# Optimization experiments

Hardware: AMD Instinct MI355X
Metric: run time of the kernel (lower is better)

Reference implementation:

```python
import jax, jax.numpy as jnp
import numpy as np

SEQ, D_IN, D_OUT = 8192, 768, 64


def setup_inputs() -> dict:
    key = jax.random.key(0)
    k0, k1, k2, k3 = jax.random.split(key, 4)
    x = jax.random.normal(k0, (SEQ, D_IN), dtype=jnp.float32)
    # nn.Linear default init ~ U(-1/sqrt(d_in), 1/sqrt(d_in)); small scale keeps softmax stable
    s = 0.02
    Wq = jax.random.normal(k1, (D_IN, D_OUT), dtype=jnp.float32) * s
    Wk = jax.random.normal(k2, (D_IN, D_OUT), dtype=jnp.float32) * s
    Wv = jax.random.normal(k3, (D_IN, D_OUT), dtype=jnp.float32) * s
    return {"x": x, "Wq": Wq, "Wk": Wk, "Wv": Wv}


def reference(x, Wq, Wk, Wv):
    # queries/keys/values: [S, d_out]
    q = x @ Wq
    k = x @ Wk
    v = x @ Wv
    d_k = k.shape[-1]
    scores = q @ k.T / jnp.sqrt(jnp.asarray(d_k, x.dtype))  # [S, S]
    weights = jax.nn.softmax(scores, axis=-1)
    return weights @ v  # [S, d_out]
```

## Files before the change

### kernel.cpp

```cpp
#include <hip/hip_runtime.h>
#include <hip/hip_bf16.h>

#define SEQ  8192
#define DIN  768
#define DOUT 64

typedef __attribute__((ext_vector_type(8))) short short8;
typedef __attribute__((ext_vector_type(4))) short s16x4;
typedef __attribute__((ext_vector_type(4))) float f32x4;

__device__ inline unsigned short f2bf(float f) {
    __hip_bfloat16 h = __float2bfloat16(f);
    return __builtin_bit_cast(unsigned short, h);
}

__global__ __launch_bounds__(256) void wconv_kernel(
    const float* __restrict__ Wq, const float* __restrict__ Wk,
    const float* __restrict__ Wv, unsigned short* __restrict__ Wf) {
    int idx = blockIdx.x * 256 + threadIdx.x;
    int c = idx / DIN;
    int k = idx - c * DIN;
    int sel = c >> 6, cc = c & 63;
    const float* W = (sel == 0) ? Wq : ((sel == 1) ? Wk : Wv);
    float v = W[k * DOUT + cc];
    if (sel == 0) v *= 0.125f * 1.4426950408889634f;
    int nt = c >> 4, l15 = c & 15;
    int kt = k >> 6, k6 = k & 63;
    int h  = k6 >> 5, r5 = k6 & 31, g = r5 >> 3, e = r5 & 7;
    Wf[(((kt * 12 + nt) * 2 + h) << 9) + (g << 7) + (l15 << 3) + e] = f2bf(v);
}

__global__ __launch_bounds__(256) void proj_kernel(
    const float* __restrict__ x, const unsigned short* __restrict__ Wf,
    unsigned short* __restrict__ Q8, unsigned short* __restrict__ Kf,
    unsigned short* __restrict__ Vf) {
    __shared__ unsigned short xs[2][16 * 72];

    const int tid  = threadIdx.x;
    const int m0   = blockIdx.x * 16;
    const int lane = tid & 63;
    const int w    = tid >> 6;
    const int g    = lane >> 4;
    const int l15  = lane & 15;
    const int sr   = tid >> 4;
    const int sc4  = (tid & 15) * 4;

    f32x4 zero = {0.f, 0.f, 0.f, 0.f};
    f32x4 acc[3] = {zero, zero, zero};

    {
        float4 f = *reinterpret_cast<const float4*>(&x[(m0 + sr) * DIN + sc4]);
        s16x4 o4;
        o4[0] = (short)f2bf(f.x); o4[1] = (short)f2bf(f.y);
        o4[2] = (short)f2bf(f.z); o4[3] = (short)f2bf(f.w);
        *(s16x4*)&xs[0][sr * 72 + sc4] = o4;
    }
    __syncthreads();

    for (int kt = 0; kt < 12; ++kt) {
        const int cur = kt & 1;
        short8 a0 = *(short8*)&xs[cur][l15 * 72 + g * 8];
        short8 a1 = *(short8*)&xs[cur][l15 * 72 + g * 8 + 32];
        if (kt + 1 < 12) {
            float4 f = *reinterpret_cast<const float4*>(
                &x[(m0 + sr) * DIN + (kt + 1) * 64 + sc4]);
            s16x4 o4;
            o4[0] = (short)f2bf(f.x); o4[1] = (short)f2bf(f.y);
            o4[2] = (short)f2bf(f.z); o4[3] = (short)f2bf(f.w);
            *(s16x4*)&xs[cur ^ 1][sr * 72 + sc4] = o4;
        }
#pragma unroll
        for (int i = 0; i < 3; ++i) {
            int nt = w * 3 + i;
            const unsigned short* wb = &Wf[((kt * 12 + nt) * 2) * 512 + lane * 8];
            short8 b0 = *(const short8*)wb;
            short8 b1 = *(const short8*)(wb + 512);
            acc[i] = __builtin_amdgcn_mfma_f32_16x16x32_bf16(a0, b0, acc[i], 0, 0, 0);
            acc[i] = __builtin_amdgcn_mfma_f32_16x16x32_bf16(a1, b1, acc[i], 0, 0, 0);
        }
        __syncthreads();
    }
#pragma unroll
    for (int i = 0; i < 3; ++i) {
#pragma unroll
        for (int r = 0; r < 4; ++r) {
            int row = m0 + g * 4 + r;
            int col = (w * 3 + i) * 16 + l15;
            unsigned short b = f2bf(acc[i][r]);
            if (col < 64) {
                Q8[row * 64 + col] = b;
            } else if (col < 128) {
                int d  = col - 64;
                int t  = row >> 6, nt = (row >> 4) & 3, lk = row & 15;
                int h  = d >> 5, kg = (d >> 3) & 3, e = d & 7;
                Kf[(((t * 4 + nt) * 2 + h) * 64 + kg * 16 + lk) * 8 + e] = b;
            } else {
                int d  = col - 128;
                int kv = row;
                int t  = kv >> 6, k6 = kv & 63;
                int c  = k6 >> 5, r5 = k6 & 31;
                int hf = r5 >> 4, vg = (r5 >> 2) & 3, j = (r5 & 3) + hf * 4;
                int dn = d >> 4, lv = d & 15;
                Vf[(((t * 2 + c) * 4 + dn) * 64 + vg * 16 + lv) * 8 + j] = b;
            }
        }
    }
}

__global__ __launch_bounds__(256, 2) void flash_kernel(
    const unsigned short* __restrict__ Q8, const unsigned short* __restrict__ Kf,
    const unsigned short* __restrict__ Vf, float* __restrict__ Op,
    float* __restrict__ Lp, int ntiles) {
    const int tid  = threadIdx.x;
    const int w    = tid >> 6;
    const int lane = tid & 63;
    const int g    = lane >> 4;
    const int l15  = lane & 15;
    const int q0   = (blockIdx.x * 4 + w) * 64;
    const int nsub = ntiles * 2;
    const int sub0 = blockIdx.y * nsub;

    short8 qa[8];
#pragma unroll
    for (int qg = 0; qg < 4; ++qg) {
        qa[qg * 2 + 0] = *(const short8*)&Q8[(q0 + qg * 16 + l15) * 64 + g * 8];
        qa[qg * 2 + 1] = *(const short8*)&Q8[(q0 + qg * 16 + l15) * 64 + g * 8 + 32];
    }

    short8 onesf;
#pragma unroll
    for (int j = 0; j < 8; ++j) onesf[j] = (short)0x3F80;

    f32x4 zero = {0.f, 0.f, 0.f, 0.f};
    f32x4 o[4][4];
    f32x4 oL[4] = {zero, zero, zero, zero};
#pragma unroll
    for (int qg = 0; qg < 4; ++qg)
#pragma unroll
        for (int dn = 0; dn < 4; ++dn) o[qg][dn] = zero;

    const unsigned short* kfp = Kf + (size_t)sub0 * 2048 + lane * 8;
    const unsigned short* vfp = Vf + (size_t)sub0 * 2048 + lane * 8;

    short8 kb[2][2], vA[4], vB[4];
#pragma unroll
    for (int nt = 0; nt < 2; ++nt)
#pragma unroll
        for (int h = 0; h < 2; ++h)
            kb[nt][h] = *(const short8*)&kfp[(nt * 2 + h) * 512];
#pragma unroll
    for (int dn = 0; dn < 4; ++dn)
        vA[dn] = *(const short8*)&vfp[dn * 512];

#define FLASH_STEP(I, VCUR, VNXT)                                                            \
    {                                                                                        \
        f32x4 s[4][2];                                                                       \
        _Pragma("unroll")                                                                    \
        for (int qg = 0; qg < 4; ++qg)                                                       \
            _Pragma("unroll")                                                                \
            for (int nt = 0; nt < 2; ++nt) s[qg][nt] = zero;                                 \
        _Pragma("unroll")                                                                    \
        for (int nt = 0; nt < 2; ++nt)                                                       \
            _Pragma("unroll")                                                                \
            for (int qg = 0; qg < 4; ++qg) {                                                 \
                s[qg][nt] = __builtin_amdgcn_mfma_f32_16x16x32_bf16(kb[nt][0], qa[qg * 2 + 0], s[qg][nt], 0, 0, 0); \
                s[qg][nt] = __builtin_amdgcn_mfma_f32_16x16x32_bf16(kb[nt][1], qa[qg * 2 + 1], s[qg][nt], 0, 0, 0); \
            }                                                                                \
        if ((I) + 1 < nsub) {                                                                \
            _Pragma("unroll")                                                                \
            for (int nt = 0; nt < 2; ++nt)                                                   \
                _Pragma("unroll")                                                            \
                for (int h = 0; h < 2; ++h)                                                  \
                    kb[nt][h] = *(const short8*)&kfp[(size_t)((I) + 1) * 2048 + (nt * 2 + h) * 512]; \
            _Pragma("unroll")                                                                \
            for (int dn = 0; dn < 4; ++dn)                                                   \
                VNXT[dn] = *(const short8*)&vfp[(size_t)((I) + 1) * 2048 + dn * 512];        \
        }                                                                                    \
        short8 pa[4];                                                                        \
        _Pragma("unroll")                                                                    \
        for (int qg = 0; qg < 4; ++qg) {                                                     \
            float p[8];                                                                      \
            _Pragma("unroll")                                                                \
            for (int nt = 0; nt < 2; ++nt)                                                   \
                _Pragma("unroll")                                                            \
                for (int r = 0; r < 4; ++r)                                                  \
                    p[nt * 4 + r] = __builtin_amdgcn_exp2f(s[qg][nt][r]);                    \
            short8 pk;                                                                       \
            _Pragma("unroll")                                                                \
            for (int j = 0; j < 8; ++j) pk[j] = (short)f2bf(p[j]);                           \
            pa[qg] = pk;                                                                     \
        }                                                                                    \
        _Pragma("unroll")                                                                    \
        for (int qg = 0; qg < 4; ++qg)                                                       \
            oL[qg] = __builtin_amdgcn_mfma_f32_16x16x32_bf16(onesf, pa[qg], oL[qg], 0, 0, 0); \
        _Pragma("unroll")                                                                    \
        for (int dn = 0; dn < 4; ++dn)                                                       \
            _Pragma("unroll")                                                                \
            for (int qg = 0; qg < 4; ++qg)                                                   \
                o[qg][dn] = __builtin_amdgcn_mfma_f32_16x16x32_bf16(VCUR[dn], pa[qg], o[qg][dn], 0, 0, 0); \
    }

    for (int i = 0; i < nsub; i += 2) {
        FLASH_STEP(i, vA, vB)
        FLASH_STEP(i + 1, vB, vA)
    }
#undef FLASH_STEP

    const size_t sb = (size_t)blockIdx.y * SEQ;
#pragma unroll
    for (int qg = 0; qg < 4; ++qg) {
#pragma unroll
        for (int dn = 0; dn < 4; ++dn)
            *(f32x4*)&Op[(sb + q0 + qg * 16 + l15) * 64 + dn * 16 + 4 * g] = o[qg][dn];
        if (g == 0) {
            Lp[sb + q0 + qg * 16 + l15] = oL[qg][0];
        }
    }
}

__global__ __launch_bounds__(256) void reduce_kernel(
    const float* __restrict__ Op, const float* __restrict__ Lp,
    float* __restrict__ Out, int NS) {
    int q  = blockIdx.x * 16 + (threadIdx.x >> 4);
    int d4 = (threadIdx.x & 15) * 4;
    float L = 0.f;
    f32x4 acc = {0.f, 0.f, 0.f, 0.f};
    for (int s = 0; s < NS; ++s) {
        L   += Lp[s * SEQ + q];
        acc += *(const f32x4*)&Op[((size_t)s * SEQ + q) * 64 + d4];
    }
    float inv = 1.0f / L;
    f32x4 r = {acc[0] * inv, acc[1] * inv, acc[2] * inv, acc[3] * inv};
    *(f32x4*)&Out[q * 64 + d4] = r;
}

extern "C" void kernel_launch(void* const* d_in, const int* in_sizes, int n_in,
                              void* d_out, int out_size, void* d_ws, size_t ws_size,
                              hipStream_t stream) {
    const float* x  = (const float*)d_in[0];
    const float* Wq = (const float*)d_in[1];
    const float* Wk = (const float*)d_in[2];
    const float* Wv = (const float*)d_in[3];
    float* out = (float*)d_out;

    char* ws = (char*)d_ws;
    unsigned short* Wf = (unsigned short*)(ws);
    unsigned short* Q8 = (unsigned short*)(ws + 294912);
    unsigned short* Kf = (unsigned short*)(ws + 294912 + 1048576);
    unsigned short* Vf = (unsigned short*)(ws + 294912 + 2097152);
    const size_t fixed = 294912 + 3 * 1048576;

    int NS = 16;
    while (NS > 1 && fixed + (size_t)NS * (2097152 + 32768) > ws_size) NS >>= 1;
    float* Op = (float*)(ws + fixed);
    float* Lp = (float*)(ws + fixed + (size_t)NS * 2097152);
    const int ntiles = SEQ / (NS * 64);

    wconv_kernel<<<dim3(576), dim3(256), 0, stream>>>(Wq, Wk, Wv, Wf);
    proj_kernel<<<dim3(512), dim3(256), 0, stream>>>(x, Wf, Q8, Kf, Vf);
    flash_kernel<<<dim3(32, NS), dim3(256), 0, stream>>>(Q8, Kf, Vf, Op, Lp, ntiles);
    reduce_kernel<<<dim3(512), dim3(256), 0, stream>>>(Op, Lp, out, NS);
}
```

Baseline: 49.29 us.

## Widen projection K-step to 128 and raise wave priority around attention MFMAs

The projection kernel now stages 128 columns of x per iteration (two float4 loads per thread, padded LDS rows of 136), halving the loop trips and barriers and issuing four MFMAs per tile per sync. The flash attention step wraps its QK and PV MFMA blocks in s_setprio(1)/s_setprio(0) so waves issuing matrix work get scheduler priority over waves doing exp/convert work. This is meant to cut barrier overhead in the projection and improve MFMA/VALU interleaving across waves. In exchange it uses more LDS and registers in the projection, and the priority hints may have no effect or reduce overlap.

```diff
diff --git a/kernel.cpp b/kernel.cpp
--- a/kernel.cpp
+++ b/kernel.cpp
@@ -34,7 +34,7 @@
     const float* __restrict__ x, const unsigned short* __restrict__ Wf,
     unsigned short* __restrict__ Q8, unsigned short* __restrict__ Kf,
     unsigned short* __restrict__ Vf) {
-    __shared__ unsigned short xs[2][16 * 72];
+    __shared__ unsigned short xs[2][16 * 136];
 
     const int tid  = threadIdx.x;
     const int m0   = blockIdx.x * 16;
@@ -43,40 +43,41 @@
     const int g    = lane >> 4;
     const int l15  = lane & 15;
     const int sr   = tid >> 4;
-    const int sc4  = (tid & 15) * 4;
+    const int sc8  = (tid & 15) * 8;
 
     f32x4 zero = {0.f, 0.f, 0.f, 0.f};
     f32x4 acc[3] = {zero, zero, zero};
 
-    {
-        float4 f = *reinterpret_cast<const float4*>(&x[(m0 + sr) * DIN + sc4]);
-        s16x4 o4;
-        o4[0] = (short)f2bf(f.x); o4[1] = (short)f2bf(f.y);
-        o4[2] = (short)f2bf(f.z); o4[3] = (short)f2bf(f.w);
-        *(s16x4*)&xs[0][sr * 72 + sc4] = o4;
-    }
+    auto stage = [&](int kk, int buf) {
+        const float4* s4 = reinterpret_cast<const float4*>(
+            &x[(m0 + sr) * DIN + kk * 128 + sc8]);
+        float4 f0 = s4[0], f1 = s4[1];
+        short8 o8;
+        o8[0]=(short)f2bf(f0.x); o8[1]=(short)f2bf(f0.y); o8[2]=(short)f2bf(f0.z); o8[3]=(short)f2bf(f0.w);
+        o8[4]=(short)f2bf(f1.x); o8[5]=(short)f2bf(f1.y); o8[6]=(short)f2bf(f1.z); o8[7]=(short)f2bf(f1.w);
+        *(short8*)&xs[buf][sr * 136 + sc8] = o8;
+    };
+
+    stage(0, 0);
     __syncthreads();
 
-    for (int kt = 0; kt < 12; ++kt) {
-        const int cur = kt & 1;
-        short8 a0 = *(short8*)&xs[cur][l15 * 72 + g * 8];
-        short8 a1 = *(short8*)&xs[cur][l15 * 72 + g * 8 + 32];
-        if (kt + 1 < 12) {
-            float4 f = *reinterpret_cast<const float4*>(
-                &x[(m0 + sr) * DIN + (kt + 1) * 64 + sc4]);
-            s16x4 o4;
-            o4[0] = (short)f2bf(f.x); o4[1] = (short)f2bf(f.y);
-            o4[2] = (short)f2bf(f.z); o4[3] = (short)f2bf(f.w);
-            *(s16x4*)&xs[cur ^ 1][sr * 72 + sc4] = o4;
-        }
+    for (int kk = 0; kk < 6; ++kk) {
+        const int buf = kk & 1;
+        short8 a00 = *(short8*)&xs[buf][l15 * 136 + g * 8];
+        short8 a01 = *(short8*)&xs[buf][l15 * 136 + g * 8 + 32];
+        short8 a10 = *(short8*)&xs[buf][l15 * 136 + g * 8 + 64];
+        short8 a11 = *(short8*)&xs[buf][l15 * 136 + g * 8 + 96];
+        if (kk + 1 < 6) stage(kk + 1, buf ^ 1);
 #pragma unroll
         for (int i = 0; i < 3; ++i) {
-            int nt = w * 3 + i;
-            const unsigned short* wb = &Wf[((kt * 12 + nt) * 2) * 512 + lane * 8];
-            short8 b0 = *(const short8*)wb;
-            short8 b1 = *(const short8*)(wb + 512);
-            acc[i] = __builtin_amdgcn_mfma_f32_16x16x32_bf16(a0, b0, acc[i], 0, 0, 0);
-            acc[i] = __builtin_amdgcn_mfma_f32_16x16x32_bf16(a1, b1, acc[i], 0, 0, 0);
+            int nt  = w * 3 + i;
+            int kt0 = 2 * kk, kt1 = 2 * kk + 1;
+            const unsigned short* wb0 = &Wf[((kt0 * 12 + nt) * 2) * 512 + lane * 8];
+            const unsigned short* wb1 = &Wf[((kt1 * 12 + nt) * 2) * 512 + lane * 8];
+            acc[i] = __builtin_amdgcn_mfma_f32_16x16x32_bf16(a00, *(const short8*)wb0,         acc[i], 0, 0, 0);
+            acc[i] = __builtin_amdgcn_mfma_f32_16x16x32_bf16(a01, *(const short8*)(wb0 + 512), acc[i], 0, 0, 0);
+            acc[i] = __builtin_amdgcn_mfma_f32_16x16x32_bf16(a10, *(const short8*)wb1,         acc[i], 0, 0, 0);
+            acc[i] = __builtin_amdgcn_mfma_f32_16x16x32_bf16(a11, *(const short8*)(wb1 + 512), acc[i], 0, 0, 0);
         }
         __syncthreads();
     }
@@ -159,6 +160,7 @@
         for (int qg = 0; qg < 4; ++qg)                                                       \
             _Pragma("unroll")                                                                \
             for (int nt = 0; nt < 2; ++nt) s[qg][nt] = zero;                                 \
+        __builtin_amdgcn_s_setprio(1);                                                       \
         _Pragma("unroll")                                                                    \
         for (int nt = 0; nt < 2; ++nt)                                                       \
             _Pragma("unroll")                                                                \
@@ -166,6 +168,7 @@
                 s[qg][nt] = __builtin_amdgcn_mfma_f32_16x16x32_bf16(kb[nt][0], qa[qg * 2 + 0], s[qg][nt], 0, 0, 0); \
                 s[qg][nt] = __builtin_amdgcn_mfma_f32_16x16x32_bf16(kb[nt][1], qa[qg * 2 + 1], s[qg][nt], 0, 0, 0); \
             }                                                                                \
+        __builtin_amdgcn_s_setprio(0);                                                       \
         if ((I) + 1 < nsub) {                                                                \
             _Pragma("unroll")                                                                \
             for (int nt = 0; nt < 2; ++nt)                                                   \
@@ -190,6 +193,7 @@
             for (int j = 0; j < 8; ++j) pk[j] = (short)f2bf(p[j]);                           \
             pa[qg] = pk;                                                                     \
         }                                                                                    \
+        __builtin_amdgcn_s_setprio(1);                                                       \
         _Pragma("unroll")                                                                    \
         for (int qg = 0; qg < 4; ++qg)                                                       \
             oL[qg] = __builtin_amdgcn_mfma_f32_16x16x32_bf16(onesf, pa[qg], oL[qg], 0, 0, 0); \
@@ -198,6 +202,7 @@
             _Pragma("unroll")                                                                \
             for (int qg = 0; qg < 4; ++qg)                                                   \
                 o[qg][dn] = __builtin_amdgcn_mfma_f32_16x16x32_bf16(VCUR[dn], pa[qg], o[qg][dn], 0, 0, 0); \
+        __builtin_amdgcn_s_setprio(0);                                                       \
     }
 
     for (int i = 0; i < nsub; i += 2) {
```

After: 49.34 us, median of 2. About the same (+0.1%).
